# Kernel optimization log

Measured on AMD Instinct MI355X. Metric: run time of the kernel, lower is better.

The kernel has to match this reference:

```python
import jax, jax.numpy as jnp
import numpy as np

EPS = 1e-6

def _complex_linear(xr, xi, wr, wi):
    # torch Linear: y = x @ W.T ; complex: (xr+i*xi)(Wr+i*Wi)
    yr = jnp.einsum('bsd,ed->bse', xr, wr) - jnp.einsum('bsd,ed->bse', xi, wi)
    yi = jnp.einsum('bsd,ed->bse', xr, wi) + jnp.einsum('bsd,ed->bse', xi, wr)
    return yr, yi

def setup_inputs() -> dict:
    key = jax.random.key(0)
    ks = jax.random.split(key, 12)
    B, S, D = 32768, 16, 64
    inp = {
        'z_real': jax.random.normal(ks[0], (B, D), jnp.float32),
        'z_imag': jax.random.normal(ks[1], (B, D), jnp.float32),
        'mem':    jax.random.normal(ks[2], (B, S, 2 * D), jnp.float32),
        'ptr':    jax.random.uniform(ks[3], (B, S), jnp.float32),
        'ctrl':   jax.random.normal(ks[4], (B, 3), jnp.float32),
        'wq_r': jax.random.normal(ks[5], (D, D), jnp.float32) / np.sqrt(D),
        'wq_i': jax.random.normal(ks[6], (D, D), jnp.float32) / np.sqrt(D),
        'wk_r': jax.random.normal(ks[7], (D, D), jnp.float32) / np.sqrt(D),
        'wk_i': jax.random.normal(ks[8], (D, D), jnp.float32) / np.sqrt(D),
        'wv_r': jax.random.normal(ks[9], (D, D), jnp.float32) / np.sqrt(D),
        'wv_i': jax.random.normal(ks[10], (D, D), jnp.float32) / np.sqrt(D),
    }
    return inp

def reference(z_real, z_imag, mem, ptr, ctrl, wq_r, wq_i, wk_r, wk_i, wv_r, wv_i):
    D = z_real.shape[-1]
    # soft push/pop/stay gates, normalized
    g = jax.nn.sigmoid(ctrl)  # (B,3)
    push, pop, stay = g[:, 0:1], g[:, 1:2], g[:, 2:3]
    total = push + pop + stay + EPS
    push, pop, stay = push / total, pop / total, stay / total
    # pointer update via rolls
    ptr_up = jnp.roll(ptr, 1, axis=1)
    ptr_down = jnp.roll(ptr, -1, axis=1)
    new_ptr = push * ptr_up + pop * ptr_down + stay * ptr  # (B,S)
    # memory write
    z_flat = jnp.concatenate([z_real, z_imag], axis=-1)  # (B,2D)
    mem_new = mem * (1.0 - push[..., None]) + push[..., None] * z_flat[:, None, :]
    mr, mi = mem_new[..., :D], mem_new[..., D:]  # (B,S,D) complex memory
    # complex attention over stack slots
    qr, qi = _complex_linear(mr, mi, wq_r, wq_i)
    kr, ki = _complex_linear(mr, mi, wk_r, wk_i)
    vr, vi = _complex_linear(mr, mi, wv_r, wv_i)
    q_flat = jnp.concatenate([qr, qi], axis=-1)  # (B,S,2D)
    k_flat = jnp.concatenate([kr, ki], axis=-1)
    scale = D ** (-0.5)
    scores = jnp.einsum('bse,bte->bst', q_flat, k_flat) * scale  # (B,S,S)
    attn = jax.nn.softmax(scores, axis=-1)
    ar = jnp.einsum('bst,btd->bsd', attn, vr)
    ai = jnp.einsum('bst,btd->bsd', attn, vi)
    att_flat = jnp.concatenate([ar, ai], axis=-1)  # (B,S,2D)
    # pointer-weighted read
    read_flat = (att_flat * new_ptr[..., None]).sum(axis=1)  # (B,2D)
    z_read_r, z_read_i = read_flat[:, :D], read_flat[:, D:]
    active_slots = (new_ptr > 0.1).astype(jnp.float32).sum(axis=1).mean()
    return (z_read_r, z_read_i, mem_new, new_ptr, active_slots)
```

## Files before the change

kernel.cpp:

```cpp
#include <hip/hip_runtime.h>


typedef __bf16 bf16x8 __attribute__((ext_vector_type(8)));
typedef float  f32x4  __attribute__((ext_vector_type(4)));
typedef float  f4     __attribute__((ext_vector_type(4)));

#define B_TOT   32768
#define GRID_WG 512
#define NWAVES  4096
#define BPW     8
#define LOG2E   1.4426950408889634f
#define EXSC    0.18033688011112042f

__device__ __forceinline__ unsigned short f2bf(float x) {
  __bf16 h = (__bf16)x;
  return __builtin_bit_cast(unsigned short, h);
}
__device__ __forceinline__ float rcp_f(float x) { return __builtin_amdgcn_rcpf(x); }
__device__ __forceinline__ float ex2_f(float x) { return __builtin_amdgcn_exp2f(x); }
__device__ __forceinline__ float sigm(float x) { return rcp_f(1.0f + ex2_f(-LOG2E * x)); }

__device__ __forceinline__ bf16x8 negbf8(bf16x8 v) {
  uint4 u = __builtin_bit_cast(uint4, v);
  u.x ^= 0x80008000u; u.y ^= 0x80008000u; u.z ^= 0x80008000u; u.w ^= 0x80008000u;
  return __builtin_bit_cast(bf16x8, u);
}

__device__ __forceinline__ float dpp_sum16(float v) {
  int x;
  x = __builtin_amdgcn_update_dpp(0, __builtin_bit_cast(int, v), 0xB1, 0xF, 0xF, false);
  v += __builtin_bit_cast(float, x);
  x = __builtin_amdgcn_update_dpp(0, __builtin_bit_cast(int, v), 0x4E, 0xF, 0xF, false);
  v += __builtin_bit_cast(float, x);
  x = __builtin_amdgcn_update_dpp(0, __builtin_bit_cast(int, v), 0x141, 0xF, 0xF, false);
  v += __builtin_bit_cast(float, x);
  x = __builtin_amdgcn_update_dpp(0, __builtin_bit_cast(int, v), 0x140, 0xF, 0xF, false);
  v += __builtin_bit_cast(float, x);
  return v;
}

__device__ __forceinline__ float dpp_ror1(float v) {
  int x = __builtin_amdgcn_update_dpp(0, __builtin_bit_cast(int, v), 0x121, 0xF, 0xF, true);
  return __builtin_bit_cast(float, x);
}
__device__ __forceinline__ float dpp_ror15(float v) {
  int x = __builtin_amdgcn_update_dpp(0, __builtin_bit_cast(int, v), 0x12F, 0xF, 0xF, true);
  return __builtin_bit_cast(float, x);
}

__global__ void ems_fin(const unsigned int* __restrict__ c, float* __restrict__ out) {
  if (threadIdx.x == 0) out[0] = (float)(*c) * (1.0f / 32768.0f);
}

__global__ void __launch_bounds__(128)
ems_mt(const float* __restrict__ wqr, const float* __restrict__ wqi,
       const float* __restrict__ wkr, const float* __restrict__ wki,
       unsigned short* __restrict__ mt, unsigned int* __restrict__ cnt)
{
  if (blockIdx.x == 0 && threadIdx.x == 0) *cnt = 0u;
  __shared__ float sK[128];
  const int e2 = (int)blockIdx.x;
  const int e  = (int)threadIdx.x;
  float kv;
  if (e < 64) kv = (e2 < 64) ? wkr[e*64 + e2]      : -wki[e*64 + (e2-64)];
  else        kv = (e2 < 64) ? wki[(e-64)*64 + e2] :  wkr[(e-64)*64 + (e2-64)];
  sK[e] = kv;
  __syncthreads();
  float acc = 0.0f;
  #pragma unroll 8
  for (int Ep = 0; Ep < 64; ++Ep) {
    float q = (e < 64) ? wqr[Ep*64 + e] : -wqi[Ep*64 + (e-64)];
    acc += q * sK[Ep];
  }
  #pragma unroll 8
  for (int Ep = 0; Ep < 64; ++Ep) {
    float q = (e < 64) ? wqi[Ep*64 + e] : wqr[Ep*64 + (e-64)];
    acc += q * sK[64 + Ep];
  }
  mt[e2*128 + e] = f2bf(acc);
}

__global__ void __launch_bounds__(512, 4)
ems_main(const float* __restrict__ z_real, const float* __restrict__ z_imag,
         const float* __restrict__ mem,    const float* __restrict__ ptrv,
         const float* __restrict__ ctrl,
         const float* __restrict__ wvr,    const float* __restrict__ wvi,
         const unsigned short* __restrict__ mt,
         float* __restrict__ out_zr, float* __restrict__ out_zi,
         float* __restrict__ out_mem, float* __restrict__ out_ptr,
         unsigned int* __restrict__ ws_cnt)
{
  __shared__ __align__(16) unsigned short lds[40960];

  const int tid = (int)threadIdx.x;

  for (int idx = tid; idx < 16384; idx += 512) {
    int e2 = idx >> 7, e = idx & 127;
    lds[(e2 << 7) + (((e >> 3) ^ (e2 & 15)) << 3) + (e & 7)] = mt[idx];
  }
  #pragma unroll
  for (int m = 0; m < 2; ++m) {
    const float* wp = m ? wvi : wvr;
    for (int idx = tid; idx < 4096; idx += 512) {
      int e = idx >> 6, d = idx & 63;
      lds[16384 + (m << 12) + (e << 6) + (((d >> 3) ^ (e & 7)) << 3) + (d & 7)] = f2bf(wp[idx]);
    }
  }
  __syncthreads();

  const int lane = tid & 63;
  const int wv   = tid >> 6;
  const int c    = lane & 15;
  const int g    = lane >> 4;
  const int d4   = lane & 31;

  {
    int phase = (wv << 1) | (((int)blockIdx.x >> 8) & 1);
    #pragma unroll 1
    for (int i = 0; i < phase; ++i) __builtin_amdgcn_s_sleep(44);
  }

  unsigned short* SY = &lds[24576 + (wv << 11)];

  const f4* mem4 = (const f4*)mem;
  const f4* zr4  = (const f4*)z_real;
  const f4* zi4  = (const f4*)z_imag;
  f4* omem4 = (f4*)out_mem;

  unsigned int active_acc = 0u;
  const int b0 = (int)blockIdx.x * 8 + wv;

  for (int it = 0; it < BPW; ++it) {
    const int b = b0 + it * NWAVES;
    const int bu = __builtin_amdgcn_readfirstlane(b);

    f4 cm[8];
    #pragma unroll
    for (int k = 0; k < 8; ++k) cm[k] = mem4[b*512 + (k << 6) + lane];
    f4 z4 = (d4 < 16) ? zr4[b*16 + d4] : zi4[b*16 + (d4 - 16)];
    float pc = ptrv[b*16 + c];

    float pu = sigm(ctrl[bu*3+0]);
    float po = sigm(ctrl[bu*3+1]);
    float st = sigm(ctrl[bu*3+2]);
    float rt = rcp_f(pu + po + st + 1e-6f);
    pu *= rt; po *= rt; st *= rt;

    float pm = dpp_ror1(pc);
    float pp = dpp_ror15(pc);
    float np = pu*pm + po*pp + st*pc;
    if (g == 0) out_ptr[b*16 + c] = np;
    unsigned long long ball = __ballot(np > 0.1f);
    active_acc += (unsigned int)__popcll(ball & 0xFFFFull);

    float om = 1.0f - pu;
    #pragma unroll
    for (int k = 0; k < 8; ++k) {
      f4 r = cm[k] * om + pu * z4;
      omem4[b*512 + (k << 6) + lane] = r;
      uint2 pk;
      pk.x = (unsigned)f2bf(r[0]) | ((unsigned)f2bf(r[1]) << 16);
      pk.y = (unsigned)f2bf(r[2]) | ((unsigned)f2bf(r[3]) << 16);
      int row = (k << 1) + (lane >> 5);
      *(uint2*)&SY[(row << 7) + (((d4 >> 1) ^ row) << 3) + ((d4 & 1) << 2)] = pk;
    }

    bf16x8 af[4], afn[2];
    #pragma unroll
    for (int t = 0; t < 4; ++t)
      af[t] = *(const bf16x8*)&SY[(c << 7) + ((((t << 2) + g) ^ c) << 3)];
    afn[0] = negbf8(af[2]);
    afn[1] = negbf8(af[3]);

    __builtin_amdgcn_s_setprio(1);
    #pragma unroll
    for (int n2 = 0; n2 < 8; ++n2) {
      int e2 = (n2 << 4) + c;
      f32x4 acc = {0.f,0.f,0.f,0.f};
      #pragma unroll
      for (int T = 0; T < 4; ++T) {
        bf16x8 am = *(const bf16x8*)&lds[(e2 << 7) + ((((T << 2) + g) ^ c) << 3)];
        acc = __builtin_amdgcn_mfma_f32_16x16x32_bf16(am, af[T], acc, 0, 0, 0);
      }
      uint2 pk;
      pk.x = (unsigned)f2bf(acc[0]) | ((unsigned)f2bf(acc[1]) << 16);
      pk.y = (unsigned)f2bf(acc[2]) | ((unsigned)f2bf(acc[3]) << 16);
      *(uint2*)&SY[(c << 7) + ((((n2 << 1) + (g >> 1)) ^ c) << 3) + ((g & 1) << 2)] = pk;
    }

    f32x4 sc = {0.f,0.f,0.f,0.f};
    #pragma unroll
    for (int T = 0; T < 4; ++T) {
      bf16x8 yb = *(const bf16x8*)&SY[(c << 7) + ((((T << 2) + g) ^ c) << 3)];
      sc = __builtin_amdgcn_mfma_f32_16x16x32_bf16(af[T], yb, sc, 0, 0, 0);
    }
    __builtin_amdgcn_s_setprio(0);

    float e0 = ex2_f(sc[0] * EXSC);
    float e1 = ex2_f(sc[1] * EXSC);
    float e2v = ex2_f(sc[2] * EXSC);
    float e3 = ex2_f(sc[3] * EXSC);
    float r = (e0 + e1) + (e2v + e3);
    r += __shfl_xor(r, 16, 64);
    r += __shfl_xor(r, 32, 64);
    float u = np * rcp_f(r);
    float w4[4];
    w4[0] = dpp_sum16(u * e0);
    w4[1] = dpp_sum16(u * e1);
    w4[2] = dpp_sum16(u * e2v);
    w4[3] = dpp_sum16(u * e3);

    __builtin_amdgcn_s_setprio(1);
    #pragma unroll
    for (int n = 0; n < 4; ++n) {
      int eb = 16384 + (((n << 4) + c) << 6);
      int e7 = c & 7;
      f32x4 ar = {0.f,0.f,0.f,0.f}, ai = {0.f,0.f,0.f,0.f};
      #pragma unroll
      for (int t = 0; t < 2; ++t) {
        int ch = (((t << 2) + g) ^ e7) << 3;
        bf16x8 fr = *(const bf16x8*)&lds[eb + ch];
        bf16x8 fi = *(const bf16x8*)&lds[eb + 4096 + ch];
        ar = __builtin_amdgcn_mfma_f32_16x16x32_bf16(af[t],   fr, ar, 0,0,0);
        ai = __builtin_amdgcn_mfma_f32_16x16x32_bf16(af[t],   fi, ai, 0,0,0);
        ar = __builtin_amdgcn_mfma_f32_16x16x32_bf16(afn[t],  fi, ar, 0,0,0);
        ai = __builtin_amdgcn_mfma_f32_16x16x32_bf16(af[t+2], fr, ai, 0,0,0);
      }
      float prr = ar[0]*w4[0] + ar[1]*w4[1] + ar[2]*w4[2] + ar[3]*w4[3];
      float pri = ai[0]*w4[0] + ai[1]*w4[1] + ai[2]*w4[2] + ai[3]*w4[3];
      prr += __shfl_xor(prr, 16, 64);
      prr += __shfl_xor(prr, 32, 64);
      pri += __shfl_xor(pri, 16, 64);
      pri += __shfl_xor(pri, 32, 64);
      if (g == 0) out_zr[b*64 + (n << 4) + c] = prr;
      if (g == 1) out_zi[b*64 + (n << 4) + c] = pri;
    }
    __builtin_amdgcn_s_setprio(0);
  }

  __syncthreads();
  unsigned int* cnt_lds = (unsigned int*)&lds[24576];
  if (tid == 0) *cnt_lds = 0u;
  __syncthreads();
  if (lane == 0) atomicAdd(cnt_lds, active_acc);
  __syncthreads();
  if (tid == 0) atomicAdd(ws_cnt, *cnt_lds);
}

extern "C" void kernel_launch(void* const* d_in, const int* in_sizes, int n_in,
                              void* d_out, int out_size, void* d_ws, size_t ws_size,
                              hipStream_t stream) {
  const float* z_real = (const float*)d_in[0];
  const float* z_imag = (const float*)d_in[1];
  const float* memp   = (const float*)d_in[2];
  const float* ptrv   = (const float*)d_in[3];
  const float* ctrl   = (const float*)d_in[4];
  const float* wq_r   = (const float*)d_in[5];
  const float* wq_i   = (const float*)d_in[6];
  const float* wk_r   = (const float*)d_in[7];
  const float* wk_i   = (const float*)d_in[8];
  const float* wv_r   = (const float*)d_in[9];
  const float* wv_i   = (const float*)d_in[10];

  float* out     = (float*)d_out;
  float* out_zr  = out;
  float* out_zi  = out + 2097152;
  float* out_mem = out + 4194304;
  float* out_ptr = out + 71303168;
  float* out_sc  = out + 71827456;

  unsigned int*   cnt = (unsigned int*)d_ws;
  unsigned short* mtp = (unsigned short*)((char*)d_ws + 1024);

  ems_mt<<<128, 128, 0, stream>>>(wq_r, wq_i, wk_r, wk_i, mtp, cnt);
  ems_main<<<GRID_WG, 512, 0, stream>>>(z_real, z_imag, memp, ptrv, ctrl,
                                        wv_r, wv_i, mtp,
                                        out_zr, out_zi, out_mem, out_ptr, cnt);
  ems_fin<<<1, 64, 0, stream>>>(cnt, out_sc);
}
```

Measured before the change: 145.0 us.

## Split memory write into a separate streaming lerp kernel before attention

Moves the mem_new blend out of the attention kernel into a standalone grid-stride streaming kernel. The attention kernel then reads the already-written mem_new back from the output buffer. This unfuses the stages so each kernel can focus on one access pattern, but it adds a second full pass of roughly 268MB of global reads. That extra traffic may hit in cache.

New measurement: 197.1 us. 36.0% more time.

```diff
diff --git a/kernel.cpp b/kernel.cpp
--- a/kernel.cpp
+++ b/kernel.cpp
@@ -80,15 +80,40 @@
   mt[e2*128 + e] = f2bf(acc);
 }
 
+__global__ void __launch_bounds__(256)
+ems_lerp(const float* __restrict__ z_real, const float* __restrict__ z_imag,
+         const float* __restrict__ mem,    const float* __restrict__ ctrl,
+         float* __restrict__ out_mem)
+{
+  const f4* mem4 = (const f4*)mem;
+  const f4* zr4  = (const f4*)z_real;
+  const f4* zi4  = (const f4*)z_imag;
+  f4* omem4 = (f4*)out_mem;
+
+  const int stride = 2048 * 256;
+  int i4 = (int)blockIdx.x * 256 + (int)threadIdx.x;
+  #pragma unroll 1
+  for (; i4 < B_TOT * 512; i4 += stride) {
+    const int b = __builtin_amdgcn_readfirstlane(i4 >> 9);
+    float pu = sigm(ctrl[b*3+0]);
+    float po = sigm(ctrl[b*3+1]);
+    float st = sigm(ctrl[b*3+2]);
+    float rt = rcp_f(pu + po + st + 1e-6f);
+    pu *= rt;
+    const int q = i4 & 511, col4 = q & 31;
+    f4 z4 = (col4 < 16) ? zr4[b*16 + col4] : zi4[b*16 + (col4 - 16)];
+    f4 r = mem4[i4] * (1.0f - pu) + pu * z4;
+    omem4[i4] = r;
+  }
+}
+
 __global__ void __launch_bounds__(512, 4)
-ems_main(const float* __restrict__ z_real, const float* __restrict__ z_imag,
-         const float* __restrict__ mem,    const float* __restrict__ ptrv,
+ems_attn(const float* __restrict__ nmem,   const float* __restrict__ ptrv,
          const float* __restrict__ ctrl,
          const float* __restrict__ wvr,    const float* __restrict__ wvi,
          const unsigned short* __restrict__ mt,
          float* __restrict__ out_zr, float* __restrict__ out_zi,
-         float* __restrict__ out_mem, float* __restrict__ out_ptr,
-         unsigned int* __restrict__ ws_cnt)
+         float* __restrict__ out_ptr, unsigned int* __restrict__ ws_cnt)
 {
   __shared__ __align__(16) unsigned short lds[40960];
 
@@ -122,10 +147,7 @@
 
   unsigned short* SY = &lds[24576 + (wv << 11)];
 
-  const f4* mem4 = (const f4*)mem;
-  const f4* zr4  = (const f4*)z_real;
-  const f4* zi4  = (const f4*)z_imag;
-  f4* omem4 = (f4*)out_mem;
+  const f4* nmem4 = (const f4*)nmem;
 
   unsigned int active_acc = 0u;
   const int b0 = (int)blockIdx.x * 8 + wv;
@@ -136,8 +158,7 @@
 
     f4 cm[8];
     #pragma unroll
-    for (int k = 0; k < 8; ++k) cm[k] = mem4[b*512 + (k << 6) + lane];
-    f4 z4 = (d4 < 16) ? zr4[b*16 + d4] : zi4[b*16 + (d4 - 16)];
+    for (int k = 0; k < 8; ++k) cm[k] = nmem4[b*512 + (k << 6) + lane];
     float pc = ptrv[b*16 + c];
 
     float pu = sigm(ctrl[bu*3+0]);
@@ -153,11 +174,9 @@
     unsigned long long ball = __ballot(np > 0.1f);
     active_acc += (unsigned int)__popcll(ball & 0xFFFFull);
 
-    float om = 1.0f - pu;
     #pragma unroll
     for (int k = 0; k < 8; ++k) {
-      f4 r = cm[k] * om + pu * z4;
-      omem4[b*512 + (k << 6) + lane] = r;
+      f4 r = cm[k];
       uint2 pk;
       pk.x = (unsigned)f2bf(r[0]) | ((unsigned)f2bf(r[1]) << 16);
       pk.y = (unsigned)f2bf(r[2]) | ((unsigned)f2bf(r[3]) << 16);
@@ -273,8 +292,9 @@
   unsigned short* mtp = (unsigned short*)((char*)d_ws + 1024);
 
   ems_mt<<<128, 128, 0, stream>>>(wq_r, wq_i, wk_r, wk_i, mtp, cnt);
-  ems_main<<<GRID_WG, 512, 0, stream>>>(z_real, z_imag, memp, ptrv, ctrl,
+  ems_lerp<<<2048, 256, 0, stream>>>(z_real, z_imag, memp, ctrl, out_mem);
+  ems_attn<<<GRID_WG, 512, 0, stream>>>(out_mem, ptrv, ctrl,
                                         wv_r, wv_i, mtp,
-                                        out_zr, out_zi, out_mem, out_ptr, cnt);
+                                        out_zr, out_zi, out_ptr, cnt);
   ems_fin<<<1, 64, 0, stream>>>(cnt, out_sc);
 }
```
